# Kernel tuning notes

Measured on AMD Instinct MI355X. Metric: run time of the kernel, lower is better.

The kernel has to match this reference:

```python
import jax, jax.numpy as jnp
import numpy as np

B, S, DIM = 2, 2048, 2048
NH = 16
Q_LORA, KV_LORA = 1536, 512
NOPE, ROPE, VHD = 128, 64, 128
QK_HD = NOPE + ROPE  # 192
EPS = 1e-6
SCALE = QK_HD ** -0.5


def rmsnorm(x, w, eps=EPS):
    return x * jax.lax.rsqrt(jnp.mean(x * x, axis=-1, keepdims=True) + eps) * w


def apply_rope(x, cos, sin):
    # x: (b, s, h, d) with d even; cos/sin: (s, d//2)
    xr, xi = x[..., 0::2], x[..., 1::2]
    c = cos[None, :, None, :]
    s = sin[None, :, None, :]
    yr = xr * c - xi * s
    yi = xr * s + xi * c
    return jnp.stack([yr, yi], axis=-1).reshape(x.shape)


def setup_inputs() -> dict:
    key = jax.random.key(0)
    ks = jax.random.split(key, 12)
    std = 0.02
    # RoPE tables (unit-magnitude complex as cos/sin)
    inv_freq = 1.0 / (10000.0 ** (np.arange(0, ROPE, 2, dtype=np.float32) / ROPE))  # (32,)
    ang = np.arange(S, dtype=np.float32)[:, None] * inv_freq[None, :]  # (S, 32)
    return {
        "x": jax.random.normal(ks[0], (B, S, DIM), jnp.float32),
        "freqs_cos": jnp.asarray(np.cos(ang)),
        "freqs_sin": jnp.asarray(np.sin(ang)),
        "wq_a_w": jax.random.normal(ks[1], (Q_LORA, DIM), jnp.float32) * std,
        "wq_a_b": jnp.zeros((Q_LORA,), jnp.float32),
        "q_norm_w": jnp.ones((Q_LORA,), jnp.float32),
        "wq_b_w": jax.random.normal(ks[2], (NH * QK_HD, Q_LORA), jnp.float32) * std,
        "wq_b_b": jnp.zeros((NH * QK_HD,), jnp.float32),
        "wkv_a_w": jax.random.normal(ks[3], (KV_LORA + ROPE, DIM), jnp.float32) * std,
        "wkv_a_b": jnp.zeros((KV_LORA + ROPE,), jnp.float32),
        "kv_norm_w": jnp.ones((KV_LORA,), jnp.float32),
        "wkv_b_w": jax.random.normal(ks[4], (NH * (NOPE + VHD), KV_LORA), jnp.float32) * std,
        "wkv_b_b": jnp.zeros((NH * (NOPE + VHD),), jnp.float32),
        "wo_w": jax.random.normal(ks[5], (DIM, NH * VHD), jnp.float32) * std,
        "wo_b": jnp.zeros((DIM,), jnp.float32),
    }


def reference(x, freqs_cos, freqs_sin, wq_a_w, wq_a_b, q_norm_w, wq_b_w, wq_b_b,
              wkv_a_w, wkv_a_b, kv_norm_w, wkv_b_w, wkv_b_b, wo_w, wo_b):
    b, s, _ = x.shape
    # Low-rank Q projection: wq_b(q_norm(wq_a(x)))
    q = rmsnorm(x @ wq_a_w.T + wq_a_b, q_norm_w) @ wq_b_w.T + wq_b_b
    q = q.reshape(b, s, NH, QK_HD)
    q_nope, q_pe = q[..., :NOPE], q[..., NOPE:]
    q = jnp.concatenate([q_nope, apply_rope(q_pe, freqs_cos, freqs_sin)], axis=-1)
    # Low-rank KV projection
    kv = x @ wkv_a_w.T + wkv_a_b  # (b, s, kv_lora + rope)
    kv_c, k_pe = kv[..., :KV_LORA], kv[..., KV_LORA:]
    k_pe = apply_rope(k_pe[:, :, None, :], freqs_cos, freqs_sin)  # (b, s, 1, rope)
    kv = rmsnorm(kv_c, kv_norm_w) @ wkv_b_w.T + wkv_b_b
    kv = kv.reshape(b, s, NH, NOPE + VHD)
    k_nope, v = kv[..., :NOPE], kv[..., NOPE:]
    k = jnp.concatenate([k_nope, jnp.broadcast_to(k_pe, (b, s, NH, ROPE))], axis=-1)
    # Causal SDPA
    scores = jnp.einsum("bqhd,bkhd->bhqk", q, k) * SCALE
    causal = jnp.tril(jnp.ones((s, s), bool))
    scores = jnp.where(causal[None, None], scores, jnp.float32(-1e30))
    attn = jax.nn.softmax(scores, axis=-1)
    out = jnp.einsum("bhqk,bkhd->bqhd", attn, v).reshape(b, s, NH * VHD)
    return out @ wo_w.T + wo_b
```

## Files before the change

### kernel.cpp

```cpp
#include <hip/hip_runtime.h>


typedef __bf16 bf16x8 __attribute__((ext_vector_type(8)));
typedef float f32x4 __attribute__((ext_vector_type(4)));
typedef unsigned short u16;

#define SEQ 2048
#define SCALE 0.07216878364870323f
#define NEGBIG -30000.0f

__device__ __forceinline__ float b2f(u16 u) {
  union { unsigned u; float f; } c; c.u = ((unsigned)u) << 16; return c.f;
}
__device__ __forceinline__ u16 f2b(float f) {
  union { float f; unsigned u; } c; c.f = f;
  unsigned r = (c.u + 0x7fffu + ((c.u >> 16) & 1u)) >> 16;
  return (u16)r;
}
__device__ __forceinline__ uint4 pack8(float4 a, float4 b) {
  union { uint4 v; u16 e[8]; } t;
  t.e[0] = f2b(a.x); t.e[1] = f2b(a.y); t.e[2] = f2b(a.z); t.e[3] = f2b(a.w);
  t.e[4] = f2b(b.x); t.e[5] = f2b(b.y); t.e[6] = f2b(b.z); t.e[7] = f2b(b.w);
  return t.v;
}

__global__ void cvt_kernel(const float* __restrict__ src, u16* __restrict__ dst,
                           long n8) {
  long i = (long)blockIdx.x * 256 + threadIdx.x;
  long stride = (long)gridDim.x * 256;
  for (; i < n8; i += stride) {
    const float4* s = (const float4*)(src + i * 8);
    float4 a = s[0], b = s[1];
    *(uint4*)(dst + i * 8) = pack8(a, b);
  }
}

template <int XF, int WF, int OF>
__global__ __launch_bounds__(256, 3) void gemm_kernel(
    const void* __restrict__ X, int lda, const void* __restrict__ W,
    const float* __restrict__ bias, void* __restrict__ out,
    int M, int N, int K, float oscale) {
  constexpr int LDT = 72;
  __shared__ alignas(16) u16 As[64 * LDT];
  __shared__ alignas(16) u16 Bs[128 * LDT];
  const int tid = threadIdx.x;
  const int wave = tid >> 6, lane = tid & 63;
  const int quad = lane >> 4, l16 = lane & 15;
  const int bm = blockIdx.x * 64, bn = blockIdx.y * 128;
  const int wn = wave * 32;
  const int srow = tid >> 3;
  const int scol = (tid & 7) * 8;

  f32x4 acc[4][2] = {};

  float4 pa32[2][2], pb32[4][2];
  uint4  pa16[2],    pb16[4];

  auto load_tile = [&](int k0) {
#pragma unroll
    for (int p = 0; p < 2; ++p) {
      size_t off = (size_t)(bm + srow + p * 32) * lda + k0 + scol;
      if (XF) {
        const float* s = (const float*)X + off;
        pa32[p][0] = *(const float4*)s;
        pa32[p][1] = *(const float4*)(s + 4);
      } else {
        pa16[p] = *(const uint4*)((const u16*)X + off);
      }
    }
#pragma unroll
    for (int p = 0; p < 4; ++p) {
      int n = bn + srow + p * 32;
      size_t off = (size_t)n * K + k0 + scol;
      if (WF) {
        if (n < N) {
          const float* s = (const float*)W + off;
          pb32[p][0] = *(const float4*)s;
          pb32[p][1] = *(const float4*)(s + 4);
        } else {
          pb32[p][0] = make_float4(0.f, 0.f, 0.f, 0.f);
          pb32[p][1] = make_float4(0.f, 0.f, 0.f, 0.f);
        }
      } else {
        if (n < N) pb16[p] = *(const uint4*)((const u16*)W + off);
        else { pb16[p].x = pb16[p].y = pb16[p].z = pb16[p].w = 0u; }
      }
    }
  };

  load_tile(0);
  for (int k0 = 0; k0 < K; k0 += 64) {
    __syncthreads();
#pragma unroll
    for (int p = 0; p < 2; ++p) {
      uint4 v;
      if (XF) v = pack8(pa32[p][0], pa32[p][1]); else v = pa16[p];
      *(uint4*)(&As[(srow + p * 32) * LDT + scol]) = v;
    }
#pragma unroll
    for (int p = 0; p < 4; ++p) {
      uint4 v;
      if (WF) v = pack8(pb32[p][0], pb32[p][1]); else v = pb16[p];
      *(uint4*)(&Bs[(srow + p * 32) * LDT + scol]) = v;
    }
    __syncthreads();
    if (k0 + 64 < K) load_tile(k0 + 64);

#pragma unroll
    for (int kk = 0; kk < 64; kk += 32) {
      bf16x8 a[4], b[2];
#pragma unroll
      for (int i = 0; i < 4; ++i)
        a[i] = *(const bf16x8*)(&As[(i * 16 + l16) * LDT + kk + quad * 8]);
#pragma unroll
      for (int j = 0; j < 2; ++j)
        b[j] = *(const bf16x8*)(&Bs[(wn + j * 16 + l16) * LDT + kk + quad * 8]);
#pragma unroll
      for (int i = 0; i < 4; ++i)
#pragma unroll
        for (int j = 0; j < 2; ++j)
          acc[i][j] = __builtin_amdgcn_mfma_f32_16x16x32_bf16(a[i], b[j], acc[i][j], 0, 0, 0);
    }
  }

#pragma unroll
  for (int i = 0; i < 4; ++i)
#pragma unroll
    for (int j = 0; j < 2; ++j) {
      int col = bn + wn + j * 16 + l16;
      if (col < N) {
        float bv = bias[col];
#pragma unroll
        for (int r = 0; r < 4; ++r) {
          int row = bm + i * 16 + quad * 4 + r;
          float v = (acc[i][j][r] + bv) * oscale;
          if (OF) ((float*)out)[(size_t)row * N + col] = v;
          else    ((u16*)out)[(size_t)row * N + col] = f2b(v);
        }
      }
    }
}

__global__ void rmsnorm_kernel(u16* x, const float* __restrict__ w,
                               int C, int stride) {
  size_t base = (size_t)blockIdx.x * stride;
  float s = 0.f;
  for (int c = threadIdx.x; c < C; c += 256) { float v = b2f(x[base + c]); s += v * v; }
#pragma unroll
  for (int off = 32; off > 0; off >>= 1) s += __shfl_xor(s, off, 64);
  __shared__ float red[4];
  if ((threadIdx.x & 63) == 0) red[threadIdx.x >> 6] = s;
  __syncthreads();
  float tot = red[0] + red[1] + red[2] + red[3];
  float scale = rsqrtf(tot / (float)C + 1e-6f);
  for (int c = threadIdx.x; c < C; c += 256)
    x[base + c] = f2b(b2f(x[base + c]) * scale * w[c]);
}

__global__ void rope_kpe_kernel(const u16* __restrict__ kvn,
                                const float* __restrict__ fcos,
                                const float* __restrict__ fsin,
                                u16* __restrict__ kpe) {
  int idx = blockIdx.x * 256 + threadIdx.x;
  int t = idx >> 5, i = idx & 31;
  int s = t & (SEQ - 1);
  float c = fcos[s * 32 + i], sn = fsin[s * 32 + i];
  float xr = b2f(kvn[(size_t)t * 576 + 512 + 2 * i]);
  float xi = b2f(kvn[(size_t)t * 576 + 512 + 2 * i + 1]);
  kpe[(size_t)t * 64 + 2 * i]     = f2b(xr * c - xi * sn);
  kpe[(size_t)t * 64 + 2 * i + 1] = f2b(xr * sn + xi * c);
}

__global__ void rope_q_kernel(u16* q, const float* __restrict__ fcos,
                              const float* __restrict__ fsin) {
  int idx = blockIdx.x * 256 + threadIdx.x;
  int t = idx >> 8, h = (idx >> 5) & 7, i = idx & 31;
  int s = t & (SEQ - 1);
  float c = fcos[s * 32 + i], sn = fsin[s * 32 + i];
  size_t base = (size_t)t * 1536 + h * 192 + 128 + 2 * i;
  float xr = b2f(q[base]), xi = b2f(q[base + 1]);
  q[base]     = f2b(xr * c - xi * sn);
  q[base + 1] = f2b(xr * sn + xi * c);
}

__global__ __launch_bounds__(256, 2) void attn_kernel(
    const u16* __restrict__ Q,
    const u16* __restrict__ KVB,
    const u16* __restrict__ KPE,
    u16* __restrict__ O,
    int hbase) {
  constexpr int LK = 200;
  constexpr int LP = 72;
  __shared__ alignas(16) u16 Ks[64 * LK];
  __shared__ alignas(16) u16 Ps[64 * LP];
  __shared__ alignas(16) u16 Vs[128 * LP];

  const int tid = threadIdx.x;
  const int wave = tid >> 6, lane = tid & 63;
  const int quad = lane >> 4, l16 = lane & 15;
  const int hl = blockIdx.y;
  const size_t tok0 = (size_t)blockIdx.z * SEQ;

  auto process = [&](int qt) {
    const int q0 = qt * 64;
    bf16x8 qf[6];
    {
      const u16* qp = Q + (tok0 + q0 + wave * 16 + l16) * 1536 + hl * 192 + quad * 8;
#pragma unroll
      for (int c = 0; c < 6; ++c) qf[c] = *(const bf16x8*)(qp + c * 32);
    }

    f32x4 o_acc[8] = {};
    float m_i[4], l_i[4];
#pragma unroll
    for (int r = 0; r < 4; ++r) { m_i[r] = NEGBIG; l_i[r] = 0.f; }

    const int nkt = qt + 1;
    uint4 kreg[6], vreg[4];
    auto load_tile = [&](int kt) {
      int k0 = kt * 64;
#pragma unroll
      for (int p = 0; p < 6; ++p) {
        int flat = tid + p * 256;
        int r = flat / 24, c8 = (flat % 24) * 8;
        const u16* src = (c8 < 128)
            ? (KVB + (tok0 + k0 + r) * 2048 + hl * 256 + c8)
            : (KPE + (tok0 + k0 + r) * 64 + (c8 - 128));
        kreg[p] = *(const uint4*)src;
      }
#pragma unroll
      for (int p = 0; p < 4; ++p) {
        int flat = tid + p * 256;
        int r = flat / 16, c8 = (flat % 16) * 8;
        vreg[p] = *(const uint4*)(KVB + (tok0 + k0 + r) * 2048 + hl * 256 + 128 + c8);
      }
    };

    load_tile(0);
    for (int kt = 0; kt < nkt; ++kt) {
      const int k0 = kt * 64;
      __syncthreads();
#pragma unroll
      for (int p = 0; p < 6; ++p) {
        int flat = tid + p * 256;
        int r = flat / 24, c8 = (flat % 24) * 8;
        *(uint4*)(&Ks[r * LK + c8]) = kreg[p];
      }
#pragma unroll
      for (int p = 0; p < 4; ++p) {
        int flat = tid + p * 256;
        int r = flat / 16, c8 = (flat % 16) * 8;
        union { uint4 v4; u16 e[8]; } t;
        t.v4 = vreg[p];
        int rs = r >> 3, rl = r & 7;
#pragma unroll
        for (int j = 0; j < 8; ++j) {
          int n = c8 + j;
          Vs[n * LP + ((rs ^ ((n >> 3) & 7)) << 3) + rl] = t.e[j];
        }
      }
      __syncthreads();
      if (kt + 1 < nkt) load_tile(kt + 1);

      f32x4 sc[4];
#pragma unroll
      for (int ni = 0; ni < 4; ++ni) {
        f32x4 a = {};
#pragma unroll
        for (int c = 0; c < 6; ++c) {
          bf16x8 kf = *(const bf16x8*)(&Ks[(ni * 16 + l16) * LK + c * 32 + quad * 8]);
          a = __builtin_amdgcn_mfma_f32_16x16x32_bf16(qf[c], kf, a, 0, 0, 0);
        }
        sc[ni] = a;
      }

      const int qrow_base = q0 + wave * 16 + quad * 4;
      if (kt == nkt - 1) {
#pragma unroll
        for (int ni = 0; ni < 4; ++ni) {
          int col = k0 + ni * 16 + l16;
#pragma unroll
          for (int r = 0; r < 4; ++r)
            if (col > qrow_base + r) sc[ni][r] = NEGBIG;
        }
      }

      float mloc[4];
#pragma unroll
      for (int r = 0; r < 4; ++r) mloc[r] = NEGBIG;
#pragma unroll
      for (int ni = 0; ni < 4; ++ni)
#pragma unroll
        for (int r = 0; r < 4; ++r) mloc[r] = fmaxf(mloc[r], sc[ni][r]);
#pragma unroll
      for (int off = 1; off < 16; off <<= 1)
#pragma unroll
        for (int r = 0; r < 4; ++r) mloc[r] = fmaxf(mloc[r], __shfl_xor(mloc[r], off, 64));

      float alpha[4], rsum[4];
#pragma unroll
      for (int r = 0; r < 4; ++r) {
        float mn = fmaxf(m_i[r], mloc[r]);
        alpha[r] = __expf(m_i[r] - mn);
        m_i[r] = mn;
        rsum[r] = 0.f;
      }
#pragma unroll
      for (int ni = 0; ni < 4; ++ni)
#pragma unroll
        for (int r = 0; r < 4; ++r) {
          float p = __expf(sc[ni][r] - m_i[r]);
          sc[ni][r] = p;
          rsum[r] += p;
        }
#pragma unroll
      for (int off = 1; off < 16; off <<= 1)
#pragma unroll
        for (int r = 0; r < 4; ++r) rsum[r] += __shfl_xor(rsum[r], off, 64);
#pragma unroll
      for (int r = 0; r < 4; ++r) l_i[r] = l_i[r] * alpha[r] + rsum[r];

#pragma unroll
      for (int ni = 0; ni < 4; ++ni)
#pragma unroll
        for (int r = 0; r < 4; ++r)
          Ps[(wave * 16 + quad * 4 + r) * LP + ni * 16 + l16] = f2b(sc[ni][r]);

      __syncthreads();

#pragma unroll
      for (int t8 = 0; t8 < 8; ++t8)
#pragma unroll
        for (int r = 0; r < 4; ++r) o_acc[t8][r] *= alpha[r];

      bf16x8 pf0 = *(const bf16x8*)(&Ps[(wave * 16 + l16) * LP + quad * 8]);
      bf16x8 pf1 = *(const bf16x8*)(&Ps[(wave * 16 + l16) * LP + 32 + quad * 8]);
#pragma unroll
      for (int ni = 0; ni < 8; ++ni) {
        int n0 = ni * 16 + l16;
        int sw = (n0 >> 3) & 7;
        bf16x8 vf0 = *(const bf16x8*)(&Vs[n0 * LP + ((quad ^ sw) << 3)]);
        bf16x8 vf1 = *(const bf16x8*)(&Vs[n0 * LP + (((4 + quad) ^ sw) << 3)]);
        o_acc[ni] = __builtin_amdgcn_mfma_f32_16x16x32_bf16(pf0, vf0, o_acc[ni], 0, 0, 0);
        o_acc[ni] = __builtin_amdgcn_mfma_f32_16x16x32_bf16(pf1, vf1, o_acc[ni], 0, 0, 0);
      }
    }

#pragma unroll
    for (int ni = 0; ni < 8; ++ni) {
      int col = (hbase + hl) * 128 + ni * 16 + l16;
#pragma unroll
      for (int r = 0; r < 4; ++r) {
        size_t row = tok0 + q0 + wave * 16 + quad * 4 + r;
        O[row * 2048 + col] = f2b(o_acc[ni][r] / l_i[r]);
      }
    }
  };

  process(blockIdx.z == 0 ? (31 - (int)blockIdx.x) : (int)blockIdx.x);
}

extern "C" void kernel_launch(void* const* d_in, const int* in_sizes, int n_in,
                              void* d_out, int out_size, void* d_ws, size_t ws_size,
                              hipStream_t stream) {
  const float* x      = (const float*)d_in[0];
  const float* fcos   = (const float*)d_in[1];
  const float* fsin   = (const float*)d_in[2];
  const float* wqa    = (const float*)d_in[3];
  const float* wqa_b  = (const float*)d_in[4];
  const float* qnw    = (const float*)d_in[5];
  const float* wqb    = (const float*)d_in[6];
  const float* wqb_b  = (const float*)d_in[7];
  const float* wkva   = (const float*)d_in[8];
  const float* wkva_b = (const float*)d_in[9];
  const float* kvnw   = (const float*)d_in[10];
  const float* wkvb   = (const float*)d_in[11];
  const float* wkvb_b = (const float*)d_in[12];
  const float* wo     = (const float*)d_in[13];
  const float* wo_b   = (const float*)d_in[14];

  char* ws = (char*)d_ws;
  u16* qn   = (u16*)(ws + 0);
  u16* kvn  = (u16*)(ws + 12582912);
  u16* kpe  = (u16*)(ws + 17301504);
  u16* qb   = (u16*)(ws + 17825792);
  u16* kvbb = (u16*)(ws + 30408704);
  u16* ao   = (u16*)(ws + 47185920);

  dim3 blk(256);

  if (ws_size >= 111411200u) {
    u16* xb    = (u16*)(ws + 63963136);
    u16* wqab  = (u16*)(ws + 80740352);
    u16* wkvab = (u16*)(ws + 87031808);
    u16* wqbb  = (u16*)(ws + 89391104);
    u16* wkvbw = (u16*)(ws + 98828288);
    u16* wob   = (u16*)(ws + 103022592);

    cvt_kernel<<<2048, blk, 0, stream>>>(x,    xb,    1048576);
    cvt_kernel<<<1536, blk, 0, stream>>>(wqa,  wqab,   393216);
    cvt_kernel<<< 576, blk, 0, stream>>>(wkva, wkvab,  147456);
    cvt_kernel<<<2048, blk, 0, stream>>>(wqb,  wqbb,   589824);
    cvt_kernel<<<1024, blk, 0, stream>>>(wkvb, wkvbw,  262144);
    cvt_kernel<<<2048, blk, 0, stream>>>(wo,   wob,    524288);

    gemm_kernel<0,0,0><<<dim3(64, 12), blk, 0, stream>>>(xb, 2048, wqab, wqa_b, qn, 4096, 1536, 2048, 1.0f);
    gemm_kernel<0,0,0><<<dim3(64, 5),  blk, 0, stream>>>(xb, 2048, wkvab, wkva_b, kvn, 4096, 576, 2048, 1.0f);
    rmsnorm_kernel<<<4096, blk, 0, stream>>>(qn, qnw, 1536, 1536);
    rmsnorm_kernel<<<4096, blk, 0, stream>>>(kvn, kvnw, 512, 576);
    rope_kpe_kernel<<<512, blk, 0, stream>>>(kvn, fcos, fsin, kpe);

    for (int g = 0; g < 2; ++g) {
      const u16* wqb_g   = wqbb + (size_t)g * 1536 * 1536;
      const float* wqb_bg  = wqb_b + g * 1536;
      const u16* wkvb_g  = wkvbw + (size_t)g * 2048 * 512;
      const float* wkvb_bg = wkvb_b + g * 2048;
      gemm_kernel<0,0,0><<<dim3(64, 12), blk, 0, stream>>>(qn, 1536, wqb_g, wqb_bg, qb, 4096, 1536, 1536, SCALE);
      rope_q_kernel<<<4096, blk, 0, stream>>>(qb, fcos, fsin);
      gemm_kernel<0,0,0><<<dim3(64, 16), blk, 0, stream>>>(kvn, 576, wkvb_g, wkvb_bg, kvbb, 4096, 2048, 512, 1.0f);
      attn_kernel<<<dim3(32, 8, 2), blk, 0, stream>>>(qb, kvbb, kpe, ao, g * 8);
    }

    gemm_kernel<0,0,1><<<dim3(64, 16), blk, 0, stream>>>(ao, 2048, wob, wo_b, (float*)d_out, 4096, 2048, 2048, 1.0f);
  } else {
    gemm_kernel<1,1,0><<<dim3(64, 12), blk, 0, stream>>>(x, 2048, wqa, wqa_b, qn, 4096, 1536, 2048, 1.0f);
    gemm_kernel<1,1,0><<<dim3(64, 5),  blk, 0, stream>>>(x, 2048, wkva, wkva_b, kvn, 4096, 576, 2048, 1.0f);
    rmsnorm_kernel<<<4096, blk, 0, stream>>>(qn, qnw, 1536, 1536);
    rmsnorm_kernel<<<4096, blk, 0, stream>>>(kvn, kvnw, 512, 576);
    rope_kpe_kernel<<<512, blk, 0, stream>>>(kvn, fcos, fsin, kpe);

    for (int g = 0; g < 2; ++g) {
      const float* wqb_g   = wqb + (size_t)g * 1536 * 1536;
      const float* wqb_bg  = wqb_b + g * 1536;
      const float* wkvb_g  = wkvb + (size_t)g * 2048 * 512;
      const float* wkvb_bg = wkvb_b + g * 2048;
      gemm_kernel<0,1,0><<<dim3(64, 12), blk, 0, stream>>>(qn, 1536, wqb_g, wqb_bg, qb, 4096, 1536, 1536, SCALE);
      rope_q_kernel<<<4096, blk, 0, stream>>>(qb, fcos, fsin);
      gemm_kernel<0,1,0><<<dim3(64, 16), blk, 0, stream>>>(kvn, 576, wkvb_g, wkvb_bg, kvbb, 4096, 2048, 512, 1.0f);
      attn_kernel<<<dim3(32, 8, 2), blk, 0, stream>>>(qb, kvbb, kpe, ao, g * 8);
    }

    gemm_kernel<0,1,1><<<dim3(64, 16), blk, 0, stream>>>(ao, 2048, wo, wo_b, (float*)d_out, 4096, 2048, 2048, 1.0f);
  }
}
```

Measured before the change: 635.6 us.

## Compute both head groups then launch a single 16-head attention kernel

```diff
diff --git a/kernel.cpp b/kernel.cpp
--- a/kernel.cpp
+++ b/kernel.cpp
@@ -184,8 +184,10 @@
 }
 
 __global__ __launch_bounds__(256, 2) void attn_kernel(
-    const u16* __restrict__ Q,
-    const u16* __restrict__ KVB,
+    const u16* __restrict__ Q0,
+    const u16* __restrict__ Q1,
+    const u16* __restrict__ KV0,
+    const u16* __restrict__ KV1,
     const u16* __restrict__ KPE,
     u16* __restrict__ O,
     int hbase) {
@@ -198,7 +200,10 @@
   const int tid = threadIdx.x;
   const int wave = tid >> 6, lane = tid & 63;
   const int quad = lane >> 4, l16 = lane & 15;
-  const int hl = blockIdx.y;
+  const int h = hbase + blockIdx.y;
+  const int hl = h & 7;
+  const u16* __restrict__ Q   = (h & 8) ? Q1  : Q0;
+  const u16* __restrict__ KVB = (h & 8) ? KV1 : KV0;
   const size_t tok0 = (size_t)blockIdx.z * SEQ;
 
   auto process = [&](int qt) {
@@ -348,7 +353,7 @@
 
 #pragma unroll
     for (int ni = 0; ni < 8; ++ni) {
-      int col = (hbase + hl) * 128 + ni * 16 + l16;
+      int col = h * 128 + ni * 16 + l16;
 #pragma unroll
       for (int r = 0; r < 4; ++r) {
         size_t row = tok0 + q0 + wave * 16 + quad * 4 + r;
@@ -383,13 +388,46 @@
   u16* qn   = (u16*)(ws + 0);
   u16* kvn  = (u16*)(ws + 12582912);
   u16* kpe  = (u16*)(ws + 17301504);
-  u16* qb   = (u16*)(ws + 17825792);
-  u16* kvbb = (u16*)(ws + 30408704);
+  u16* qbA  = (u16*)(ws + 17825792);
+  u16* kvB  = (u16*)(ws + 30408704);
   u16* ao   = (u16*)(ws + 47185920);
 
   dim3 blk(256);
 
-  if (ws_size >= 111411200u) {
+  if (ws_size >= 123994112u) {
+    u16* xb    = (u16*)(ws + 63963136);
+    u16* kvA   = (u16*)(ws + 63963136);
+    u16* wqab  = (u16*)(ws + 80740352);
+    u16* wkvab = (u16*)(ws + 87031808);
+    u16* wqbb  = (u16*)(ws + 89391104);
+    u16* wkvbw = (u16*)(ws + 98828288);
+    u16* wob   = (u16*)(ws + 103022592);
+    u16* qbB   = (u16*)(ws + 111411200);
+
+    cvt_kernel<<<2048, blk, 0, stream>>>(x,    xb,    1048576);
+    cvt_kernel<<<1536, blk, 0, stream>>>(wqa,  wqab,   393216);
+    cvt_kernel<<< 576, blk, 0, stream>>>(wkva, wkvab,  147456);
+    cvt_kernel<<<2048, blk, 0, stream>>>(wqb,  wqbb,   589824);
+    cvt_kernel<<<1024, blk, 0, stream>>>(wkvb, wkvbw,  262144);
+    cvt_kernel<<<2048, blk, 0, stream>>>(wo,   wob,    524288);
+
+    gemm_kernel<0,0,0><<<dim3(64, 12), blk, 0, stream>>>(xb, 2048, wqab, wqa_b, qn, 4096, 1536, 2048, 1.0f);
+    gemm_kernel<0,0,0><<<dim3(64, 5),  blk, 0, stream>>>(xb, 2048, wkvab, wkva_b, kvn, 4096, 576, 2048, 1.0f);
+    rmsnorm_kernel<<<4096, blk, 0, stream>>>(qn, qnw, 1536, 1536);
+    rmsnorm_kernel<<<4096, blk, 0, stream>>>(kvn, kvnw, 512, 576);
+    rope_kpe_kernel<<<512, blk, 0, stream>>>(kvn, fcos, fsin, kpe);
+
+    gemm_kernel<0,0,0><<<dim3(64, 12), blk, 0, stream>>>(qn, 1536, wqbb, wqb_b, qbA, 4096, 1536, 1536, SCALE);
+    gemm_kernel<0,0,0><<<dim3(64, 12), blk, 0, stream>>>(qn, 1536, wqbb + (size_t)1536 * 1536, wqb_b + 1536, qbB, 4096, 1536, 1536, SCALE);
+    rope_q_kernel<<<4096, blk, 0, stream>>>(qbA, fcos, fsin);
+    rope_q_kernel<<<4096, blk, 0, stream>>>(qbB, fcos, fsin);
+    gemm_kernel<0,0,0><<<dim3(64, 16), blk, 0, stream>>>(kvn, 576, wkvbw, wkvb_b, kvA, 4096, 2048, 512, 1.0f);
+    gemm_kernel<0,0,0><<<dim3(64, 16), blk, 0, stream>>>(kvn, 576, wkvbw + (size_t)2048 * 512, wkvb_b + 2048, kvB, 4096, 2048, 512, 1.0f);
+
+    attn_kernel<<<dim3(32, 16, 2), blk, 0, stream>>>(qbA, qbB, kvA, kvB, kpe, ao, 0);
+
+    gemm_kernel<0,0,1><<<dim3(64, 16), blk, 0, stream>>>(ao, 2048, wob, wo_b, (float*)d_out, 4096, 2048, 2048, 1.0f);
+  } else if (ws_size >= 111411200u) {
     u16* xb    = (u16*)(ws + 63963136);
     u16* wqab  = (u16*)(ws + 80740352);
     u16* wkvab = (u16*)(ws + 87031808);
@@ -415,10 +453,10 @@
       const float* wqb_bg  = wqb_b + g * 1536;
       const u16* wkvb_g  = wkvbw + (size_t)g * 2048 * 512;
       const float* wkvb_bg = wkvb_b + g * 2048;
-      gemm_kernel<0,0,0><<<dim3(64, 12), blk, 0, stream>>>(qn, 1536, wqb_g, wqb_bg, qb, 4096, 1536, 1536, SCALE);
-      rope_q_kernel<<<4096, blk, 0, stream>>>(qb, fcos, fsin);
-      gemm_kernel<0,0,0><<<dim3(64, 16), blk, 0, stream>>>(kvn, 576, wkvb_g, wkvb_bg, kvbb, 4096, 2048, 512, 1.0f);
-      attn_kernel<<<dim3(32, 8, 2), blk, 0, stream>>>(qb, kvbb, kpe, ao, g * 8);
+      gemm_kernel<0,0,0><<<dim3(64, 12), blk, 0, stream>>>(qn, 1536, wqb_g, wqb_bg, qbA, 4096, 1536, 1536, SCALE);
+      rope_q_kernel<<<4096, blk, 0, stream>>>(qbA, fcos, fsin);
+      gemm_kernel<0,0,0><<<dim3(64, 16), blk, 0, stream>>>(kvn, 576, wkvb_g, wkvb_bg, kvB, 4096, 2048, 512, 1.0f);
+      attn_kernel<<<dim3(32, 8, 2), blk, 0, stream>>>(qbA, qbA, kvB, kvB, kpe, ao, g * 8);
     }
 
     gemm_kernel<0,0,1><<<dim3(64, 16), blk, 0, stream>>>(ao, 2048, wob, wo_b, (float*)d_out, 4096, 2048, 2048, 1.0f);
@@ -434,10 +472,10 @@
       const float* wqb_bg  = wqb_b + g * 1536;
       const float* wkvb_g  = wkvb + (size_t)g * 2048 * 512;
       const float* wkvb_bg = wkvb_b + g * 2048;
-      gemm_kernel<0,1,0><<<dim3(64, 12), blk, 0, stream>>>(qn, 1536, wqb_g, wqb_bg, qb, 4096, 1536, 1536, SCALE);
-      rope_q_kernel<<<4096, blk, 0, stream>>>(qb, fcos, fsin);
-      gemm_kernel<0,1,0><<<dim3(64, 16), blk, 0, stream>>>(kvn, 576, wkvb_g, wkvb_bg, kvbb, 4096, 2048, 512, 1.0f);
-      attn_kernel<<<dim3(32, 8, 2), blk, 0, stream>>>(qb, kvbb, kpe, ao, g * 8);
+      gemm_kernel<0,1,0><<<dim3(64, 12), blk, 0, stream>>>(qn, 1536, wqb_g, wqb_bg, qbA, 4096, 1536, 1536, SCALE);
+      rope_q_kernel<<<4096, blk, 0, stream>>>(qbA, fcos, fsin);
+      gemm_kernel<0,1,0><<<dim3(64, 16), blk, 0, stream>>>(kvn, 576, wkvb_g, wkvb_bg, kvB, 4096, 2048, 512, 1.0f);
+      attn_kernel<<<dim3(32, 8, 2), blk, 0, stream>>>(qbA, qbA, kvB, kvB, kpe, ao, g * 8);
     }
 
     gemm_kernel<0,1,1><<<dim3(64, 16), blk, 0, stream>>>(ao, 2048, wo, wo_b, (float*)d_out, 4096, 2048, 2048, 1.0f);
```

Measured after the change: 661.8 us. +4.1%, slower.
